# Optimization experiments

Hardware: AMD Instinct MI355X
Metric: run time of the kernel (lower is better)

## Reference

```python
import jax, jax.numpy as jnp
import numpy as np
from jax import lax

B, LEN_SEQ, D_MODEL, N_HEAD, FACTOR, D_FF = 16, 512, 512, 8, 5, 2048
EPS = 1e-5


def layer_norm(x):
    mu = x.mean(-1, keepdims=True)
    var = ((x - mu) ** 2).mean(-1, keepdims=True)
    return (x - mu) * lax.rsqrt(var + EPS)


def pos_encode(x):
    pos = jnp.arange(LEN_SEQ, dtype=jnp.float32)[:, None]
    div = jnp.exp(jnp.arange(0, D_MODEL, 2, dtype=jnp.float32) * (-np.log(10000.0) / D_MODEL))
    pe = jnp.zeros((LEN_SEQ, D_MODEL))
    pe = pe.at[:, 0::2].set(jnp.sin(pos * div)).at[:, 1::2].set(jnp.cos(pos * div))
    return x + pe[None]


def prob_attention(Q, K, V, rkey):
    # Q,K,V: [B,H,L,D]; Informer ProbSparse attention, mask_flag=False
    Bq, H, L_Q, D = Q.shape
    L_K = K.shape[2]
    U_part = min(FACTOR * int(np.ceil(np.log(L_K))), L_K)   # sampled keys per query
    u = min(FACTOR * int(np.ceil(np.log(L_Q))), L_Q)        # top queries kept
    idx = jax.random.randint(rkey, (L_Q, U_part), 0, L_K)
    K_samp = K[:, :, idx, :]                                # [B,H,L_Q,U_part,D]
    QK_samp = jnp.einsum('bhld,bhlsd->bhls', Q, K_samp)
    M = QK_samp.max(-1) - QK_samp.sum(-1) / L_K             # sparsity measure
    _, top = lax.top_k(M, u)                                # [B,H,u]
    Q_red = jnp.take_along_axis(Q, top[..., None], axis=2)  # [B,H,u,D]
    scores = jnp.einsum('bhud,bhkd->bhuk', Q_red, K) * (1.0 / np.sqrt(D))
    upd = jnp.einsum('bhuk,bhkd->bhud', jax.nn.softmax(scores, -1), V)
    ctx = jnp.broadcast_to(V.mean(2, keepdims=True), (Bq, H, L_Q, D))
    bi = jnp.arange(Bq)[:, None, None]
    hi = jnp.arange(H)[None, :, None]
    return ctx.at[bi, hi, top].set(upd)


def setup_inputs():
    key = jax.random.key(0)
    ks = jax.random.split(key, 12)
    s = 0.02
    d, f = D_MODEL, D_FF
    n = jax.random.normal
    return {
        'input_data': n(ks[0], (B, LEN_SEQ, d), jnp.float32),
        'Wq': n(ks[1], (d, d)) * s, 'bq': jnp.zeros((d,)),
        'Wk': n(ks[2], (d, d)) * s, 'bk': jnp.zeros((d,)),
        'Wv': n(ks[3], (d, d)) * s, 'bv': jnp.zeros((d,)),
        'Wo': n(ks[4], (d, d)) * s, 'bo': jnp.zeros((d,)),
        'enc_w1': n(ks[5], (d, f)) * s, 'enc_b1': jnp.zeros((f,)),
        'enc_w2': n(ks[6], (f, d)) * s, 'enc_b2': jnp.zeros((d,)),
        'dec_w1': n(ks[7], (d, f)) * s, 'dec_b1': jnp.zeros((f,)),
        'dec_w2': n(ks[8], (f, d)) * s, 'dec_b2': jnp.zeros((d,)),
        'dist_w': n(ks[9], (d, d, 3)) * s, 'dist_b': jnp.zeros((d,)),
        'out_w': n(ks[10], (d, 1)) * s, 'out_b': jnp.zeros((1,)),
    }


def reference(input_data, Wq, bq, Wk, bk, Wv, bv, Wo, bo,
              enc_w1, enc_b1, enc_w2, enc_b2,
              dec_w1, dec_b1, dec_w2, dec_b2,
              dist_w, dist_b, out_w, out_b):
    base = jax.random.key(42)

    def attn(q_in, k_in, v_in, i):
        Bq, L, _ = q_in.shape
        S = k_in.shape[1]
        Q = (q_in @ Wq + bq).reshape(Bq, L, N_HEAD, -1).transpose(0, 2, 1, 3)
        K = (k_in @ Wk + bk).reshape(Bq, S, N_HEAD, -1).transpose(0, 2, 1, 3)
        V = (v_in @ Wv + bv).reshape(Bq, S, N_HEAD, -1).transpose(0, 2, 1, 3)
        ctx = prob_attention(Q, K, V, jax.random.fold_in(base, i))
        return ctx.transpose(0, 2, 1, 3).reshape(Bq, L, -1) @ Wo + bo

    def encoder(x, i):
        x = layer_norm(x + attn(x, x, x, i))
        y = jax.nn.relu(x @ enc_w1 + enc_b1) @ enc_w2 + enc_b2
        return layer_norm(x + y)

    def distill(x):  # conv1d(circular) + batchnorm + ELU + maxpool(3,2,1)
        xc = x.transpose(0, 2, 1)                                   # [B,d,L]
        xp = jnp.concatenate([xc[..., -1:], xc, xc[..., :1]], -1)   # circular pad
        y = lax.conv_general_dilated(xp, dist_w, (1,), 'VALID',
                                     dimension_numbers=('NCH', 'OIH', 'NCH'))
        y = y + dist_b[None, :, None]
        mu = y.mean((0, 2), keepdims=True)
        var = ((y - mu) ** 2).mean((0, 2), keepdims=True)
        y = jax.nn.elu((y - mu) * lax.rsqrt(var + EPS))
        y = lax.reduce_window(y, -jnp.inf, lax.max, (1, 1, 3), (1, 1, 2),
                              [(0, 0), (0, 0), (1, 1)])
        return y.transpose(0, 2, 1)

    enc_inp = pos_encode(input_data)
    dec_inp = pos_encode(input_data)
    e = distill(encoder(enc_inp, 0))   # 512 -> 256
    e = distill(encoder(e, 1))         # 256 -> 128
    e = distill(encoder(e, 2))         # 128 -> 64
    # decoder (source DecoderLayer never applies its norms; dropout = identity in eval)
    out1 = dec_inp + attn(dec_inp, dec_inp, dec_inp, 3)
    out2 = out1 + attn(out1, e, e, 4)
    y = jax.nn.relu(out2 @ dec_w1 + dec_b1) @ dec_w2 + dec_b2
    out3 = y + out2
    return out3 @ out_w + out_b
```

## Files before the change

### kernel.cpp

```cpp
#include <hip/hip_runtime.h>
#include <cstdint>
#include <cmath>


#define HD __host__ __device__

typedef short short8 __attribute__((ext_vector_type(8)));
typedef float float4v __attribute__((ext_vector_type(4)));

typedef __attribute__((address_space(1))) const void gvoid;
typedef __attribute__((address_space(3))) void lvoid;

__device__ __forceinline__ void gl_lds16(const void* g, void* l) {
    __builtin_amdgcn_global_load_lds((gvoid*)g, (lvoid*)l, 16, 0, 0);
}

__device__ inline short f2bf(float f) {
    unsigned u = __float_as_uint(f);
    unsigned r = u + 0x7FFFu + ((u >> 16) & 1u);
    return (short)(r >> 16);
}

HD inline unsigned rotl32(unsigned x, int r) { return (x << r) | (x >> (32 - r)); }
HD inline void tfround(unsigned& x0, unsigned& x1, int r) {
    x0 += x1; x1 = rotl32(x1, r); x1 ^= x0;
}
HD inline void threefry2x32(unsigned k0, unsigned k1, unsigned c0, unsigned c1,
                            unsigned& o0, unsigned& o1) {
    unsigned ks2 = k0 ^ k1 ^ 0x1BD11BDAu;
    unsigned x0 = c0 + k0, x1 = c1 + k1;
    tfround(x0, x1, 13); tfround(x0, x1, 15); tfround(x0, x1, 26); tfround(x0, x1, 6);
    x0 += k1; x1 += ks2 + 1u;
    tfround(x0, x1, 17); tfround(x0, x1, 29); tfround(x0, x1, 16); tfround(x0, x1, 24);
    x0 += ks2; x1 += k0 + 2u;
    tfround(x0, x1, 13); tfround(x0, x1, 15); tfround(x0, x1, 26); tfround(x0, x1, 6);
    x0 += k0; x1 += k1 + 3u;
    tfround(x0, x1, 17); tfround(x0, x1, 29); tfround(x0, x1, 16); tfround(x0, x1, 24);
    x0 += k1; x1 += ks2 + 4u;
    tfround(x0, x1, 13); tfround(x0, x1, 15); tfround(x0, x1, 26); tfround(x0, x1, 6);
    x0 += ks2; x1 += k0 + 5u;
    o0 = x0; o1 = x1;
}


__global__ void pe_add_k(const float* __restrict__ in, float* __restrict__ out,
                         short* __restrict__ outb, int total8) {
    int t = blockIdx.x * 256 + threadIdx.x;
    if (t >= total8) return;
    int e = t * 8;
    int d0 = e & 511;
    int l = (e >> 9) & 511;
    float4 v0 = *(const float4*)(in + e);
    float4 v1 = *(const float4*)(in + e + 4);
    float vin[8] = {v0.x, v0.y, v0.z, v0.w, v1.x, v1.y, v1.z, v1.w};
    float r[8];
    #pragma unroll
    for (int p = 0; p < 4; p++) {
        int d = d0 + 2 * p;
        float div = expf((float)d * (-0.017988946039016f));
        float ang = (float)l * div;
        float s, c;
        sincosf(ang, &s, &c);
        r[2 * p] = vin[2 * p] + s;
        r[2 * p + 1] = vin[2 * p + 1] + c;
    }
    *(float4*)(out + e) = (float4){r[0], r[1], r[2], r[3]};
    *(float4*)(out + e + 4) = (float4){r[4], r[5], r[6], r[7]};
    short8 ob;
    #pragma unroll
    for (int p = 0; p < 8; p++) ob[p] = f2bf(r[p]);
    *(short8*)(outb + e) = ob;
}

__global__ __launch_bounds__(256) void wprep_k(
    const float* __restrict__ Wq, const float* __restrict__ Wk,
    const float* __restrict__ Wv, const float* __restrict__ Wo,
    const float* __restrict__ ew1, const float* __restrict__ ew2,
    const float* __restrict__ dw1, const float* __restrict__ dw2,
    short* __restrict__ WqkvT, short* __restrict__ WoT,
    short* __restrict__ e1T, short* __restrict__ e2T,
    short* __restrict__ d1T, short* __restrict__ d2T,
    const float* __restrict__ DW, short* __restrict__ W2T,
    const float* __restrict__ b0, const float* __restrict__ b1,
    const float* __restrict__ b2, float* __restrict__ bqkv) {
    int b = blockIdx.x;
    if (b < 5120) {
        const float* in; short* out; int K, N, tb;
        if (b < 1024) {
            int w = b >> 8; tb = b & 255;
            in = (w == 0) ? Wq : (w == 1) ? Wk : (w == 2) ? Wv : Wo;
            out = (w < 3) ? WqkvT + w * 512 * 512 : WoT;
            K = 512; N = 512;
        } else if (b < 2048) { in = ew1; out = e1T; K = 512; N = 2048; tb = b - 1024; }
        else if (b < 3072)   { in = ew2; out = e2T; K = 2048; N = 512; tb = b - 2048; }
        else if (b < 4096)   { in = dw1; out = d1T; K = 512; N = 2048; tb = b - 3072; }
        else                 { in = dw2; out = d2T; K = 2048; N = 512; tb = b - 4096; }
        int nbx = N >> 5;
        int k0 = (tb / nbx) << 5, n0 = (tb % nbx) << 5;
        __shared__ float tile[32][33];
        int c = threadIdx.x & 31, r0 = threadIdx.x >> 5;
        for (int rr = r0; rr < 32; rr += 8)
            tile[rr][c] = in[(size_t)(k0 + rr) * N + n0 + c];
        __syncthreads();
        for (int rr = r0; rr < 32; rr += 8)
            out[(size_t)(n0 + rr) * K + k0 + c] = f2bf(tile[c][rr]);
        return;
    }
    if (b < 8192) {
        int t = (b - 5120) * 256 + threadIdx.x;
        int kk = t % 1536;
        int o = t / 1536;
        int h = kk / 512, i = kk % 512;
        W2T[t] = f2bf(DW[(size_t)o * 1536 + i * 3 + h]);
        return;
    }
    int t = (b - 8192) * 256 + threadIdx.x;
    if (t < 1536)
        bqkv[t] = (t < 512) ? b0[t] : (t < 1024 ? b1[t - 512] : b2[t - 1024]);
}

__device__ inline void swizzle_bid(int bid, int nbx, int nby, int& bm, int& bn) {
    if ((nby & 7) == 0) {
        int stripe = nby >> 3;
        int x = bid & 7, w = bid >> 3;
        bn = w % nbx;
        bm = x * stripe + w / nbx;
    } else {
        bn = bid % nbx;
        bm = bid / nbx;
    }
}

__global__ __launch_bounds__(256) void gemm128_k(
    const short* __restrict__ A, const short* __restrict__ Bt,
    const float* __restrict__ bias, const float* __restrict__ res,
    float* __restrict__ C32, short* __restrict__ C16,
    int M, int N, int K, int relu, int ldC) {
    __shared__ short As[2][128 * 64];
    __shared__ short Bs[2][128 * 64];
    int tid = threadIdx.x;
    int wave = tid >> 6, lane = tid & 63;
    int wy = wave >> 1, wx = wave & 1;
    int rl = lane & 15, quad = lane >> 4;
    int bm, bn;
    swizzle_bid(blockIdx.x, N >> 7, M >> 7, bm, bn);
    bm <<= 7; bn <<= 7;

    int srow = (wave << 5) + (lane >> 2);
    int skol = (((lane & 3) ^ ((srow >> 1) & 3)) << 3);
    const short* ga0 = A + (size_t)(bm + srow) * K + skol;
    const short* ga1 = ga0 + (size_t)16 * K;
    const short* gb0 = Bt + (size_t)(bn + srow) * K + skol;
    const short* gb1 = gb0 + (size_t)16 * K;
    int lao = wave << 10;
    int ksw = (quad ^ ((rl >> 1) & 3)) << 3;

    float4v acc[4][4];
    #pragma unroll
    for (int i = 0; i < 4; i++)
        #pragma unroll
        for (int j = 0; j < 4; j++) acc[i][j] = (float4v){0.f, 0.f, 0.f, 0.f};

    int niter = K >> 6;
    auto stagePair = [&](int p, int bf) {
        int k0 = p << 6;
        gl_lds16(ga0 + k0, &As[bf][lao]);
        gl_lds16(ga1 + k0, &As[bf][lao + 512]);
        gl_lds16(gb0 + k0, &Bs[bf][lao]);
        gl_lds16(gb1 + k0, &Bs[bf][lao + 512]);
        gl_lds16(ga0 + k0 + 32, &As[bf][4096 + lao]);
        gl_lds16(ga1 + k0 + 32, &As[bf][4096 + lao + 512]);
        gl_lds16(gb0 + k0 + 32, &Bs[bf][4096 + lao]);
        gl_lds16(gb1 + k0 + 32, &Bs[bf][4096 + lao + 512]);
    };
    stagePair(0, 0);
    asm volatile("s_waitcnt vmcnt(0)" ::: "memory");
    __builtin_amdgcn_s_barrier();
    __builtin_amdgcn_sched_barrier(0);
    int cur = 0;
    for (int p = 0; p < niter; ++p) {
        if (p + 1 < niter) stagePair(p + 1, cur ^ 1);
        #pragma unroll
        for (int hh = 0; hh < 2; hh++) {
            const short* Ab = &As[cur][hh * 4096];
            const short* Bb = &Bs[cur][hh * 4096];
            short8 a[4], b[4];
            #pragma unroll
            for (int i = 0; i < 4; i++)
                a[i] = *(const short8*)&Ab[(wy * 64 + i * 16 + rl) * 32 + ksw];
            #pragma unroll
            for (int j = 0; j < 4; j++)
                b[j] = *(const short8*)&Bb[(wx * 64 + j * 16 + rl) * 32 + ksw];
            #pragma unroll
            for (int i = 0; i < 4; i++)
                #pragma unroll
                for (int j = 0; j < 4; j++)
                    acc[i][j] = __builtin_amdgcn_mfma_f32_16x16x32_bf16(a[i], b[j], acc[i][j], 0, 0, 0);
        }
        asm volatile("s_waitcnt vmcnt(0)" ::: "memory");
        __builtin_amdgcn_s_barrier();
        __builtin_amdgcn_sched_barrier(0);
        cur ^= 1;
    }
    #pragma unroll
    for (int i = 0; i < 4; i++) {
        #pragma unroll
        for (int r = 0; r < 4; r++) {
            int gm = bm + wy * 64 + i * 16 + quad * 4 + r;
            #pragma unroll
            for (int j = 0; j < 4; j++) {
                int gn = bn + wx * 64 + j * 16 + rl;
                float v = acc[i][j][r];
                if (bias) v += bias[gn];
                if (relu) v = fmaxf(v, 0.f);
                if (res) v += res[(size_t)gm * ldC + gn];
                if (C32) C32[(size_t)gm * ldC + gn] = v;
                if (C16) C16[(size_t)gm * ldC + gn] = f2bf(v);
            }
        }
    }
}

extern __shared__ short gls[];

__global__ __launch_bounds__(256) void gemm12864_k(
    const short* __restrict__ A, const short* __restrict__ Bt,
    const float* __restrict__ bias, const float* __restrict__ res,
    float* __restrict__ C32, short* __restrict__ C16,
    int M, int N, int K, int relu, int ldC) {
    int tid = threadIdx.x;
    int wave = tid >> 6, lane = tid & 63;
    int wy = wave >> 1, wx = wave & 1;
    int rl = lane & 15, quad = lane >> 4;
    int bm, bn;
    swizzle_bid(blockIdx.x, N >> 6, M >> 7, bm, bn);
    bm <<= 7; bn <<= 6;

    int arow = (wave << 5) + (lane >> 2);
    int brow = (wave << 4) + (lane >> 2);
    int ska = (((lane & 3) ^ ((arow >> 1) & 3)) << 3);
    int skb = (((lane & 3) ^ ((brow >> 1) & 3)) << 3);
    const short* ga0 = A + (size_t)(bm + arow) * K + ska;
    const short* ga1 = ga0 + (size_t)16 * K;
    const short* gb0 = Bt + (size_t)(bn + brow) * K + skb;
    int lao = wave << 10;
    int lbo = wave << 9;
    int ksw = (quad ^ ((rl >> 1) & 3)) << 3;

    float4v acc[4][2];
    #pragma unroll
    for (int i = 0; i < 4; i++)
        #pragma unroll
        for (int j = 0; j < 2; j++) acc[i][j] = (float4v){0.f, 0.f, 0.f, 0.f};

    int nt = K >> 5;
    int niter = nt >> 1;

    auto stageT = [&](int t, int bf) {
        int k0 = t << 5;
        short* Ab = gls + bf * 6144;
        short* Bb = Ab + 4096;
        gl_lds16(ga0 + k0, Ab + lao);
        gl_lds16(ga1 + k0, Ab + lao + 512);
        gl_lds16(gb0 + k0, Bb + lbo);
    };
    auto computeT = [&](int bf) {
        const short* Ab = gls + bf * 6144;
        const short* Bb = Ab + 4096;
        short8 a[4], b[2];
        #pragma unroll
        for (int i = 0; i < 4; i++)
            a[i] = *(const short8*)&Ab[(wy * 64 + i * 16 + rl) * 32 + ksw];
        #pragma unroll
        for (int j = 0; j < 2; j++)
            b[j] = *(const short8*)&Bb[(wx * 32 + j * 16 + rl) * 32 + ksw];
        #pragma unroll
        for (int i = 0; i < 4; i++)
            #pragma unroll
            for (int j = 0; j < 2; j++)
                acc[i][j] = __builtin_amdgcn_mfma_f32_16x16x32_bf16(a[i], b[j], acc[i][j], 0, 0, 0);
    };

    stageT(0, 0); stageT(1, 1);
    stageT(2, 2); stageT(3, 3);
    asm volatile("s_waitcnt vmcnt(6)" ::: "memory");
    __builtin_amdgcn_s_barrier();
    __builtin_amdgcn_sched_barrier(0);
    int q = 0;
    for (int p = 0; p < niter; ++p) {
        if (p + 2 < niter) {
            int s = q + 2; if (s >= 3) s -= 3;
            int t0 = (p + 2) << 1;
            stageT(t0, 2 * s);
            stageT(t0 + 1, 2 * s + 1);
        }
        computeT(2 * q);
        computeT(2 * q + 1);
        if (p + 2 < niter) {
            asm volatile("s_waitcnt vmcnt(6)" ::: "memory");
        } else {
            asm volatile("s_waitcnt vmcnt(0)" ::: "memory");
        }
        __builtin_amdgcn_s_barrier();
        __builtin_amdgcn_sched_barrier(0);
        q = (q == 2) ? 0 : q + 1;
    }
    #pragma unroll
    for (int i = 0; i < 4; i++) {
        #pragma unroll
        for (int r = 0; r < 4; r++) {
            int gm = bm + wy * 64 + i * 16 + quad * 4 + r;
            #pragma unroll
            for (int j = 0; j < 2; j++) {
                int gn = bn + wx * 32 + j * 16 + rl;
                float v = acc[i][j][r];
                if (bias) v += bias[gn];
                if (relu) v = fmaxf(v, 0.f);
                if (res) v += res[(size_t)gm * ldC + gn];
                if (C32) C32[(size_t)gm * ldC + gn] = v;
                if (C16) C16[(size_t)gm * ldC + gn] = f2bf(v);
            }
        }
    }
}

__global__ __launch_bounds__(256) void gemm64_k(
    const short* __restrict__ A, const short* __restrict__ Bt,
    const float* __restrict__ bias, const float* __restrict__ res,
    float* __restrict__ C32, short* __restrict__ C16,
    int M, int N, int K, int relu, int ldC) {
    __shared__ short As[2][64 * 32];
    __shared__ short Bs[2][64 * 32];
    int tid = threadIdx.x;
    int wave = tid >> 6, lane = tid & 63;
    int rl = lane & 15, quad = lane >> 4;
    int bm, bn;
    swizzle_bid(blockIdx.x, N >> 6, M >> 6, bm, bn);
    bm <<= 6; bn <<= 6;

    int srow = (wave << 4) + (lane >> 2);
    int skol = (((lane & 3) ^ ((srow >> 1) & 3)) << 3);
    const short* ga = A + (size_t)(bm + srow) * K + skol;
    const short* gb = Bt + (size_t)(bn + srow) * K + skol;
    int lof = wave << 9;
    int ksw = (quad ^ ((rl >> 1) & 3)) << 3;

    float4v acc[4];
    #pragma unroll
    for (int j = 0; j < 4; j++) acc[j] = (float4v){0.f, 0.f, 0.f, 0.f};

    int nsteps = K >> 5;
    auto stage = [&](int t, int bf) {
        int k0 = t << 5;
        gl_lds16(ga + k0, &As[bf][lof]);
        gl_lds16(gb + k0, &Bs[bf][lof]);
    };
    stage(0, 0);
    asm volatile("s_waitcnt vmcnt(0)" ::: "memory");
    __builtin_amdgcn_s_barrier();
    __builtin_amdgcn_sched_barrier(0);
    int cur = 0;
    for (int t = 0; t < nsteps; ++t) {
        if (t + 1 < nsteps) stage(t + 1, cur ^ 1);
        short8 a = *(const short8*)&As[cur][(wave * 16 + rl) * 32 + ksw];
        short8 b[4];
        #pragma unroll
        for (int j = 0; j < 4; j++)
            b[j] = *(const short8*)&Bs[cur][(j * 16 + rl) * 32 + ksw];
        #pragma unroll
        for (int j = 0; j < 4; j++)
            acc[j] = __builtin_amdgcn_mfma_f32_16x16x32_bf16(a, b[j], acc[j], 0, 0, 0);
        asm volatile("s_waitcnt vmcnt(0)" ::: "memory");
        __builtin_amdgcn_s_barrier();
        __builtin_amdgcn_sched_barrier(0);
        cur ^= 1;
    }
    #pragma unroll
    for (int r = 0; r < 4; r++) {
        int gm = bm + wave * 16 + quad * 4 + r;
        #pragma unroll
        for (int j = 0; j < 4; j++) {
            int gn = bn + j * 16 + rl;
            float v = acc[j][r];
            if (bias) v += bias[gn];
            if (relu) v = fmaxf(v, 0.f);
            if (res) v += res[(size_t)gm * ldC + gn];
            if (C32) C32[(size_t)gm * ldC + gn] = v;
            if (C16) C16[(size_t)gm * ldC + gn] = f2bf(v);
        }
    }
}

__global__ void ridx_k(unsigned k0, unsigned k1, int size, unsigned mask, int* __restrict__ idx) {
    int j = blockIdx.x * 256 + threadIdx.x;
    if (j >= size) return;
    unsigned o0, o1;
    threefry2x32(k0, k1, (unsigned)j, (unsigned)(j + size), o0, o1);
    idx[j] = (int)(o1 & mask);
}

extern __shared__ float kslab[];
__global__ __launch_bounds__(256) void msamp_lds_k(
    const float* __restrict__ Qp, const float* __restrict__ Kp,
    const int* __restrict__ idx, float* __restrict__ Mout,
    int LQ, int LK, int U, int ld) {
    int bid = blockIdx.x;
    int half = bid & 1;
    int bh = bid >> 1;
    int h = bh & 7, b = bh >> 3;
    const float* kbase = Kp + (size_t)b * LK * ld + h * 64;
    for (int t = threadIdx.x; t < LK * 16; t += 256) {
        int r = t >> 4, seg = t & 15;
        float4 v = *(const float4*)(kbase + (size_t)r * ld + seg * 4);
        float* dst = &kslab[r * 65 + seg * 4];
        dst[0] = v.x; dst[1] = v.y; dst[2] = v.z; dst[3] = v.w;
    }
    __syncthreads();
    int halfL = LQ >> 1;
    for (int li = threadIdx.x; li < halfL; li += 256) {
        int l = half * halfL + li;
        const float4* q = (const float4*)(Qp + (size_t)(b * LQ + l) * ld + h * 64);
        float qr[64];
        #pragma unroll
        for (int d4 = 0; d4 < 16; d4++) {
            float4 v = q[d4];
            qr[4 * d4] = v.x; qr[4 * d4 + 1] = v.y; qr[4 * d4 + 2] = v.z; qr[4 * d4 + 3] = v.w;
        }
        const int* ip = idx + l * U;
        float mx = -INFINITY, sm = 0.f;
        for (int s = 0; s < U; s++) {
            const float* kr = &kslab[ip[s] * 65];
            float acc = 0.f;
            #pragma unroll
            for (int d = 0; d < 64; d++) acc += qr[d] * kr[d];
            mx = fmaxf(mx, acc);
            sm += acc;
        }
        Mout[(size_t)bh * LQ + l] = mx - sm / (float)LK;
    }
}

__global__ void msamp_k(const float* __restrict__ Qp, const float* __restrict__ Kp,
                        const int* __restrict__ idx, float* __restrict__ Mout,
                        int LQ, int LK, int U, int ld) {
    int t = blockIdx.x * 256 + threadIdx.x;
    int total = 16 * 8 * LQ * 4;
    if (t >= total) return;
    int p = t & 3;
    int rest = t >> 2;
    int l = rest % LQ;
    int h = (rest / LQ) & 7;
    int b = rest / (LQ * 8);
    const float4* q = (const float4*)(Qp + ((size_t)(b * LQ + l) * ld + h * 64));
    const float* kb = Kp + ((size_t)b * LK * ld + h * 64);
    float4 qr[16];
    #pragma unroll
    for (int d = 0; d < 16; d++) qr[d] = q[d];
    float mx = -INFINITY, sm = 0.f;
    for (int s = p; s < U; s += 4) {
        const float4* kr = (const float4*)(kb + (size_t)idx[l * U + s] * ld);
        float acc = 0.f;
        #pragma unroll
        for (int d = 0; d < 16; d++) {
            float4 kv = kr[d];
            acc += qr[d].x * kv.x + qr[d].y * kv.y + qr[d].z * kv.z + qr[d].w * kv.w;
        }
        mx = fmaxf(mx, acc);
        sm += acc;
    }
    mx = fmaxf(mx, __shfl_xor(mx, 1));
    mx = fmaxf(mx, __shfl_xor(mx, 2));
    sm += __shfl_xor(sm, 1);
    sm += __shfl_xor(sm, 2);
    if (p == 0)
        Mout[(size_t)((b * 8) + h) * LQ + l] = mx - sm / (float)LK;
}

__global__ __launch_bounds__(256) void topk_k(const float* __restrict__ M,
                                              int* __restrict__ top, int LQ, int u) {
    int wave = threadIdx.x >> 6, lane = threadIdx.x & 63;
    int bh = blockIdx.x * 4 + wave;
    const float* m = M + (size_t)bh * LQ;
    float v[8];
    int id[8];
    #pragma unroll
    for (int s = 0; s < 8; s++) {
        int l = s * 64 + lane;
        if (l < LQ) { v[s] = m[l]; id[s] = l; }
        else        { v[s] = -INFINITY; id[s] = 0x7FFFFFFF; }
    }
    int* o = top + bh * u;
    for (int j = 0; j < u; j++) {
        float bv = v[0]; int bi = id[0];
        #pragma unroll
        for (int s = 1; s < 8; s++)
            if (v[s] > bv || (v[s] == bv && id[s] < bi)) { bv = v[s]; bi = id[s]; }
        #pragma unroll
        for (int off = 32; off > 0; off >>= 1) {
            float v2 = __shfl_xor(bv, off);
            int i2 = __shfl_xor(bi, off);
            if (v2 > bv || (v2 == bv && i2 < bi)) { bv = v2; bi = i2; }
        }
        if (lane == 0) o[j] = bi;
        int ws = bi >> 6, wl = bi & 63;
        #pragma unroll
        for (int s = 0; s < 8; s++)
            if (s == ws && lane == wl) v[s] = -INFINITY;
    }
}

__global__ __launch_bounds__(256) void vmean_k(const float* __restrict__ Vp,
                                               float* __restrict__ vm, int LK, int ld) {
    __shared__ float red[8][33];
    int b = blockIdx.y;
    int c0 = blockIdx.x * 32;
    int ci = threadIdx.x & 31, g = threadIdx.x >> 5;
    const float* base = Vp + (size_t)b * LK * ld + c0 + ci;
    float s = 0.f;
    for (int l = g; l < LK; l += 8) s += base[(size_t)l * ld];
    red[g][ci] = s;
    __syncthreads();
    if (threadIdx.x < 32) {
        float t = 0.f;
        #pragma unroll
        for (int g2 = 0; g2 < 8; g2++) t += red[g2][threadIdx.x];
        vm[b * 512 + c0 + threadIdx.x] = t / (float)LK;
    }
}

__global__ void ctx_fill_k(const float* __restrict__ vm, short* __restrict__ ctxb,
                           int LQ, int total8) {
    int t = blockIdx.x * 256 + threadIdx.x;
    if (t >= total8) return;
    int e = t * 8;
    int c = e & 511;
    int b = e / (LQ << 9);
    float4 v0 = *(const float4*)(vm + b * 512 + c);
    float4 v1 = *(const float4*)(vm + b * 512 + c + 4);
    float vv[8] = {v0.x, v0.y, v0.z, v0.w, v1.x, v1.y, v1.z, v1.w};
    short8 ob;
    #pragma unroll
    for (int p = 0; p < 8; p++) ob[p] = f2bf(vv[p]);
    *(short8*)(ctxb + e) = ob;
}

__global__ __launch_bounds__(256) void attn_flash_k(
    const float* __restrict__ Qp, const float* __restrict__ Kp, const float* __restrict__ Vp,
    const int* __restrict__ top, short* __restrict__ ctxb, int LQ, int LK, int u, int ld) {
    __shared__ float qs[18][64];
    __shared__ int ls[18];
    __shared__ float kv[64][65];
    __shared__ float sc[18][512];
    int bid = blockIdx.x;
    int chunk = bid & 1;
    int h = (bid >> 1) & 7;
    int b = bid >> 4;
    int CH = (u + 1) >> 1;
    int r0 = chunk * CH;
    int nr = min(CH, u - r0);
    int tid = threadIdx.x;
    int wave = tid >> 6, lane = tid & 63;

    if (tid < nr) ls[tid] = top[((b * 8) + h) * u + r0 + tid];
    __syncthreads();
    for (int t = tid; t < nr * 16; t += 256) {
        int r = t >> 4, seg = t & 15;
        float4 v = *(const float4*)(Qp + ((size_t)(b * LQ + ls[r])) * ld + h * 64 + seg * 4);
        float* dst = &qs[r][seg * 4];
        dst[0] = v.x; dst[1] = v.y; dst[2] = v.z; dst[3] = v.w;
    }

    int ntile = LK >> 6;
    const float* kbase = Kp + ((size_t)b * LK) * ld + h * 64;
    for (int T = 0; T < ntile; T++) {
        __syncthreads();
        #pragma unroll
        for (int it = 0; it < 4; it++) {
            int t = tid + it * 256;
            int kk = t >> 4, seg = t & 15;
            float4 v = *(const float4*)(kbase + (size_t)(T * 64 + kk) * ld + seg * 4);
            float* dst = &kv[kk][seg * 4];
            dst[0] = v.x; dst[1] = v.y; dst[2] = v.z; dst[3] = v.w;
        }
        __syncthreads();
        for (int p = tid; p < nr * 64; p += 256) {
            int r = p >> 6, kk = p & 63;
            float acc = 0.f;
            #pragma unroll
            for (int d = 0; d < 64; d++) acc += qs[r][d] * kv[kk][d];
            sc[r][T * 64 + kk] = acc * 0.125f;
        }
    }
    __syncthreads();
    for (int r = wave; r < nr; r += 4) {
        float mx = -INFINITY;
        for (int k = lane; k < LK; k += 64) mx = fmaxf(mx, sc[r][k]);
        #pragma unroll
        for (int o = 32; o > 0; o >>= 1) mx = fmaxf(mx, __shfl_xor(mx, o));
        float s = 0.f;
        for (int k = lane; k < LK; k += 64) {
            float e = expf(sc[r][k] - mx);
            sc[r][k] = e;
            s += e;
        }
        #pragma unroll
        for (int o = 32; o > 0; o >>= 1) s += __shfl_xor(s, o);
        float inv = 1.0f / s;
        for (int k = lane; k < LK; k += 64) sc[r][k] *= inv;
    }
    float acc[5];
    #pragma unroll
    for (int i = 0; i < 5; i++) acc[i] = 0.f;
    const float* vbase = Vp + ((size_t)b * LK) * ld + h * 64;
    for (int T = 0; T < ntile; T++) {
        __syncthreads();
        #pragma unroll
        for (int it = 0; it < 4; it++) {
            int t = tid + it * 256;
            int kk = t >> 4, seg = t & 15;
            float4 v = *(const float4*)(vbase + (size_t)(T * 64 + kk) * ld + seg * 4);
            float* dst = &kv[kk][seg * 4];
            dst[0] = v.x; dst[1] = v.y; dst[2] = v.z; dst[3] = v.w;
        }
        __syncthreads();
        int ri = 0;
        for (int r = wave; r < nr; r += 4, ri++) {
            float a = 0.f;
            #pragma unroll
            for (int kk = 0; kk < 64; kk++) a += sc[r][T * 64 + kk] * kv[kk][lane];
            acc[ri] += a;
        }
    }
    int ri = 0;
    for (int r = wave; r < nr; r += 4, ri++)
        ctxb[((size_t)(b * LQ + ls[r])) * 512 + h * 64 + lane] = f2bf(acc[ri]);
}

__global__ __launch_bounds__(256) void ln_k(const float* __restrict__ in,
                                            float* __restrict__ out, short* __restrict__ outb) {
    __shared__ float wred[8];
    int r = blockIdx.x;
    int tid = threadIdx.x;
    int wave = tid >> 6, lane = tid & 63;
    const float* x = in + (size_t)r * 512;
    float a = x[tid], b = x[tid + 256];
    float s = a + b;
    #pragma unroll
    for (int o = 32; o > 0; o >>= 1) s += __shfl_xor(s, o);
    if (lane == 0) wred[wave] = s;
    __syncthreads();
    float mu = (wred[0] + wred[1] + wred[2] + wred[3]) * (1.f / 512.f);
    float d1 = a - mu, d2 = b - mu;
    float q = d1 * d1 + d2 * d2;
    #pragma unroll
    for (int o = 32; o > 0; o >>= 1) q += __shfl_xor(q, o);
    if (lane == 0) wred[wave + 4] = q;
    __syncthreads();
    float inv = 1.0f / sqrtf((wred[4] + wred[5] + wred[6] + wred[7]) * (1.f / 512.f) + 1e-5f);
    float v1 = d1 * inv, v2 = d2 * inv;
    out[(size_t)r * 512 + tid] = v1;
    out[(size_t)r * 512 + tid + 256] = v2;
    if (outb) {
        outb[(size_t)r * 512 + tid] = f2bf(v1);
        outb[(size_t)r * 512 + tid + 256] = f2bf(v2);
    }
}

__global__ void xcat_k(const float* __restrict__ x, short* __restrict__ xc, int L, int total8) {
    int t = blockIdx.x * 256 + threadIdx.x;
    if (t >= total8) return;
    int e = t * 8;
    int i = e & 511;
    int q = e >> 9;
    int h = q % 3;
    int bt = q / 3;
    int tt = bt % L;
    int b = bt / L;
    int src = (tt + h - 1 + L) % L;
    const float* s = x + (size_t)(b * L + src) * 512 + i;
    float4 v0 = *(const float4*)s;
    float4 v1 = *(const float4*)(s + 4);
    float vv[8] = {v0.x, v0.y, v0.z, v0.w, v1.x, v1.y, v1.z, v1.w};
    short8 ob;
    #pragma unroll
    for (int p = 0; p < 8; p++) ob[p] = f2bf(vv[p]);
    *(short8*)(xc + e) = ob;
}

__global__ __launch_bounds__(256) void bnpart_k(const float* __restrict__ y,
                                                float* __restrict__ ps, float* __restrict__ pq,
                                                int rows) {
    int chunk = blockIdx.x;
    int rpc = rows >> 8;
    int r0 = chunk * rpc;
    int tid = threadIdx.x;
    float s0 = 0.f, s1 = 0.f, q0 = 0.f, q1 = 0.f;
    for (int r = r0; r < r0 + rpc; r++) {
        float a = y[(size_t)r * 512 + tid];
        float b = y[(size_t)r * 512 + tid + 256];
        s0 += a; q0 += a * a;
        s1 += b; q1 += b * b;
    }
    ps[chunk * 512 + tid] = s0;
    ps[chunk * 512 + tid + 256] = s1;
    pq[chunk * 512 + tid] = q0;
    pq[chunk * 512 + tid + 256] = q1;
}

__global__ void bnfin_k(const float* __restrict__ ps, const float* __restrict__ pq,
                        float* __restrict__ mu, float* __restrict__ var, int rows) {
    int o = blockIdx.x * 256 + threadIdx.x;
    if (o >= 512) return;
    float s = 0.f, q = 0.f;
    for (int c = 0; c < 256; c++) {
        s += ps[c * 512 + o];
        q += pq[c * 512 + o];
    }
    float m = s / (float)rows;
    mu[o] = m;
    var[o] = q / (float)rows - m * m;
}

__global__ void elu_pool_k(const float* __restrict__ y, const float* __restrict__ mu,
                           const float* __restrict__ var, float* __restrict__ out,
                           short* __restrict__ outb, int L, int total8) {
    int t = blockIdx.x * 256 + threadIdx.x;
    if (t >= total8) return;
    int e = t * 8;
    int o = e & 511;
    int tp = (e >> 9) % (L / 2);
    int b = (e >> 9) / (L / 2);
    float4 m0 = *(const float4*)(mu + o);
    float4 m1 = *(const float4*)(mu + o + 4);
    float4 g0 = *(const float4*)(var + o);
    float4 g1 = *(const float4*)(var + o + 4);
    float mm[8] = {m0.x, m0.y, m0.z, m0.w, m1.x, m1.y, m1.z, m1.w};
    float gg[8] = {g0.x, g0.y, g0.z, g0.w, g1.x, g1.y, g1.z, g1.w};
    float best[8];
    #pragma unroll
    for (int p = 0; p < 8; p++) best[p] = -INFINITY;
    #pragma unroll
    for (int dt = 0; dt < 3; dt++) {
        int tt = 2 * tp - 1 + dt;
        if (tt < 0 || tt >= L) continue;
        const float* row = y + (size_t)(b * L + tt) * 512 + o;
        float4 r0 = *(const float4*)row;
        float4 r1 = *(const float4*)(row + 4);
        float rr[8] = {r0.x, r0.y, r0.z, r0.w, r1.x, r1.y, r1.z, r1.w};
        #pragma unroll
        for (int p = 0; p < 8; p++) best[p] = fmaxf(best[p], rr[p]);
    }
    float res[8];
    short8 ob;
    #pragma unroll
    for (int p = 0; p < 8; p++) {
        float m = (best[p] - mm[p]) / sqrtf(gg[p] + 1e-5f);
        float r = m > 0.f ? m : expm1f(m);
        res[p] = r;
        ob[p] = f2bf(r);
    }
    *(float4*)(out + e) = (float4){res[0], res[1], res[2], res[3]};
    *(float4*)(out + e + 4) = (float4){res[4], res[5], res[6], res[7]};
    *(short8*)(outb + e) = ob;
}

__global__ void final_k(const float* __restrict__ x, const float* __restrict__ w,
                        const float* __restrict__ bb, float* __restrict__ out, int rows) {
    int gid = blockIdx.x * 256 + threadIdx.x;
    int wid = gid >> 6;
    int lane = gid & 63;
    if (wid >= rows) return;
    const float* xr = x + (size_t)wid * 512;
    float acc = 0.f;
    for (int k = lane; k < 512; k += 64) acc += xr[k] * w[k];
    for (int off = 32; off > 0; off >>= 1) acc += __shfl_down(acc, off);
    if (lane == 0) out[wid] = acc + bb[0];
}


static inline int iceil_log(int L) { return (int)ceil(log((double)L)); }
static inline int imin(int a, int b) { return a < b ? a : b; }

extern "C" void kernel_launch(void* const* d_in, const int* in_sizes, int n_in,
                              void* d_out, int out_size, void* d_ws, size_t ws_size,
                              hipStream_t stream) {
    const float* IN  = (const float*)d_in[0];
    const float* Wq  = (const float*)d_in[1];
    const float* bq  = (const float*)d_in[2];
    const float* Wk  = (const float*)d_in[3];
    const float* bk  = (const float*)d_in[4];
    const float* Wv  = (const float*)d_in[5];
    const float* bv  = (const float*)d_in[6];
    const float* Wo  = (const float*)d_in[7];
    const float* bo  = (const float*)d_in[8];
    const float* ew1 = (const float*)d_in[9];
    const float* eb1 = (const float*)d_in[10];
    const float* ew2 = (const float*)d_in[11];
    const float* eb2 = (const float*)d_in[12];
    const float* dw1 = (const float*)d_in[13];
    const float* db1 = (const float*)d_in[14];
    const float* dw2 = (const float*)d_in[15];
    const float* db2 = (const float*)d_in[16];
    const float* DW  = (const float*)d_in[17];
    const float* db  = (const float*)d_in[18];
    const float* ow  = (const float*)d_in[19];
    const float* ob  = (const float*)d_in[20];
    float* OUT = (float*)d_out;

    float* ws = (float*)d_ws;
    size_t off = 0;
    auto alloc = [&](size_t n) { float* p = ws + off; off += n; return p; };
    float* PE   = alloc(4194304);
    short* PEb  = (short*)alloc(2097152);
    float* QKV  = alloc(12582912);
    float* CTX  = alloc(4194304);
    short* CTXb = (short*)alloc(2097152);
    float* T1   = alloc(4194304);
    short* T1b  = (short*)alloc(2097152);
    float* XLN  = alloc(4194304);
    short* XLNb = (short*)alloc(2097152);
    float* T2   = alloc(4194304);
    short* T2b  = (short*)alloc(2097152);
    float* T3   = alloc(4194304);
    short* HIDb = (short*)alloc(8388608);
    float* D1   = alloc(2097152);
    short* D1b  = (short*)alloc(1048576);
    float* D2   = alloc(1048576);
    short* D2b  = (short*)alloc(524288);
    short* Ebb  = (short*)alloc(262144);
    float* Ebf  = alloc(524288);
    float* MB   = alloc(65536);
    float* VM   = alloc(8192);
    float* MU   = alloc(512);
    float* VARb = alloc(512);
    float* BQKV = alloc(1536);
    float* PS   = alloc(131072);
    float* PQ   = alloc(131072);
    int* IDX  = (int*)alloc(17920);
    int* TOPB = (int*)alloc(4480);
    short* WqkvT = (short*)alloc(393216);
    short* WoT   = (short*)alloc(131072);
    short* ew1T  = (short*)alloc(524288);
    short* ew2T  = (short*)alloc(524288);
    short* dw1T  = (short*)alloc(524288);
    short* dw2T  = (short*)alloc(524288);
    short* W2T   = (short*)alloc(393216);
    (void)ws_size; (void)n_in; (void)in_sizes; (void)out_size;

    static_assert(512 * 65 * 4 == 133120, "");
    hipError_t attr_ok = hipFuncSetAttribute(
        (const void*)msamp_lds_k, hipFuncAttributeMaxDynamicSharedMemorySize, 133120);
    hipError_t attr_g = hipFuncSetAttribute(
        (const void*)gemm12864_k, hipFuncAttributeMaxDynamicSharedMemorySize, 73728);

    auto gemm128 = [&](const short* A, const short* Bt, const float* bias, const float* res,
                       float* C32, short* C16, int M, int N, int K, int relu, int ldC) {
        gemm128_k<<<(N / 128) * (M / 128), 256, 0, stream>>>(A, Bt, bias, res, C32, C16,
                                                             M, N, K, relu, ldC);
    };
    auto gemm64 = [&](const short* A, const short* Bt, const float* bias, const float* res,
                      float* C32, short* C16, int M, int N, int K, int relu, int ldC) {
        if (attr_g == hipSuccess && M >= 8192 && (M & 127) == 0 && (N & 63) == 0 &&
            (K & 63) == 0) {
            gemm12864_k<<<(N / 64) * (M / 128), 256, 73728, stream>>>(A, Bt, bias, res,
                                                                      C32, C16, M, N, K,
                                                                      relu, ldC);
        } else {
            gemm64_k<<<(N / 64) * (M / 64), 256, 0, stream>>>(A, Bt, bias, res, C32, C16,
                                                              M, N, K, relu, ldC);
        }
    };

    auto attn = [&](const short* qinb, const short* kvinb, const float* resp,
                    float* out32, short* out16, int LQ, int LK, int ikey) {
        int Mq = 16 * LQ, Mk = 16 * LK;
        const int ld = 1536;
        float* Qp = QKV;
        float* Kp = QKV + 512;
        float* Vp = QKV + 1024;
        if (qinb == kvinb) {
            gemm128(qinb, WqkvT, BQKV, nullptr, QKV, nullptr, Mq, 1536, 512, 0, ld);
        } else {
            gemm64(qinb, WqkvT, BQKV, nullptr, QKV, nullptr, Mq, 512, 512, 0, ld);
            gemm64(kvinb, WqkvT + 512 * 512, BQKV + 512, nullptr, QKV + 512, nullptr,
                   Mk, 1024, 512, 0, ld);
        }
        int U = imin(5 * iceil_log(LK), LK);
        int u = imin(5 * iceil_log(LQ), LQ);
        unsigned rk0, rk1;
        threefry2x32(0u, 42u, 0u, (unsigned)ikey, rk0, rk1);
        int size = LQ * U;
        ridx_k<<<(size + 255) / 256, 256, 0, stream>>>(rk0, rk1, size, (unsigned)(LK - 1), IDX);
        size_t shbytes = (size_t)LK * 65 * 4;
        if (attr_ok == hipSuccess || shbytes <= 65536) {
            msamp_lds_k<<<16 * 8 * 2, 256, shbytes, stream>>>(Qp, Kp, IDX, MB, LQ, LK, U, ld);
        } else {
            int totM = 16 * 8 * LQ * 4;
            msamp_k<<<(totM + 255) / 256, 256, 0, stream>>>(Qp, Kp, IDX, MB, LQ, LK, U, ld);
        }
        topk_k<<<32, 256, 0, stream>>>(MB, TOPB, LQ, u);
        vmean_k<<<dim3(16, 16), 256, 0, stream>>>(Vp, VM, LK, ld);
        int totC8 = 16 * LQ * 512 / 8;
        ctx_fill_k<<<(totC8 + 255) / 256, 256, 0, stream>>>(VM, CTXb, LQ, totC8);
        attn_flash_k<<<16 * 8 * 2, 256, 0, stream>>>(Qp, Kp, Vp, TOPB, CTXb, LQ, LK, u, ld);
        gemm64(CTXb, WoT, bo, resp, out32, out16, Mq, 512, 512, 0, 512);
    };

    auto encoder = [&](const short* Xb, const float* X, int L, int ikey, float* OUTenc) {
        int M = 16 * L;
        attn(Xb, Xb, X, T1, nullptr, L, L, ikey);
        ln_k<<<M, 256, 0, stream>>>(T1, XLN, XLNb);
        gemm128(XLNb, ew1T, eb1, nullptr, nullptr, HIDb, M, 2048, 512, 1, 2048);
        gemm64(HIDb, ew2T, eb2, XLN, T2, nullptr, M, 512, 2048, 0, 512);
        ln_k<<<M, 256, 0, stream>>>(T2, OUTenc, nullptr);
    };

    auto distill = [&](const float* X, int L, float* OUTd, short* OUTdb) {
        int M = 16 * L;
        int tot8 = M * 1536 / 8;
        xcat_k<<<(tot8 + 255) / 256, 256, 0, stream>>>(X, HIDb, L, tot8);
        gemm64(HIDb, W2T, db, nullptr, CTX, nullptr, M, 512, 1536, 0, 512);
        bnpart_k<<<256, 256, 0, stream>>>(CTX, PS, PQ, M);
        bnfin_k<<<2, 256, 0, stream>>>(PS, PQ, MU, VARb, M);
        int toto8 = 16 * (L / 2) * 512 / 8;
        elu_pool_k<<<(toto8 + 255) / 256, 256, 0, stream>>>(CTX, MU, VARb, OUTd, OUTdb, L, toto8);
    };

    wprep_k<<<8198, 256, 0, stream>>>(Wq, Wk, Wv, Wo, ew1, ew2, dw1, dw2,
                                      WqkvT, WoT, ew1T, ew2T, dw1T, dw2T,
                                      DW, W2T, bq, bk, bv, BQKV);

    int totPE8 = 16 * 512 * 512 / 8;
    pe_add_k<<<(totPE8 + 255) / 256, 256, 0, stream>>>(IN, PE, PEb, totPE8);

    encoder(PEb, PE, 512, 0, T3); distill(T3, 512, D1, D1b);
    encoder(D1b, D1, 256, 1, T3); distill(T3, 256, D2, D2b);
    encoder(D2b, D2, 128, 2, T3); distill(T3, 128, Ebf, Ebb);

    attn(PEb, PEb, PE, T1, T1b, 512, 512, 3);
    attn(T1b, Ebb, T1, T2, T2b, 512, 64, 4);
    gemm128(T2b, dw1T, db1, nullptr, nullptr, HIDb, 8192, 2048, 512, 1, 2048);
    gemm64(HIDb, dw2T, db2, T2, T3, nullptr, 8192, 512, 2048, 0, 512);
    final_k<<<(8192 * 64) / 256, 256, 0, stream>>>(T3, ow, ob, OUT, 8192);
}
```

Before: 1.444 ms.

## Double-buffer K/V tiles in attention kernel and split dot-product accumulators

The attention kernel now double-buffers its K and V tiles in dynamic shared memory, prefetching the next tile into registers while the current one is computed. This is meant to hide global load latency behind the score and PV loops. Dot products in both the attention and sampled-score kernels are split into four independent accumulators to shorten the FMA dependency chain, which changes float summation order. Shared memory use grows to about 75KB per block, which may lower occupancy.

Result: slower. 1.534 ms (+6.2%).

```diff
diff --git a/kernel.cpp b/kernel.cpp
--- a/kernel.cpp
+++ b/kernel.cpp
@@ -222,6 +222,7 @@
 }
 
 extern __shared__ short gls[];
+extern __shared__ float kslab[];
 
 __global__ __launch_bounds__(256) void gemm12864_k(
     const short* __restrict__ A, const short* __restrict__ Bt,
@@ -399,7 +400,6 @@
     idx[j] = (int)(o1 & mask);
 }
 
-extern __shared__ float kslab[];
 __global__ __launch_bounds__(256) void msamp_lds_k(
     const float* __restrict__ Qp, const float* __restrict__ Kp,
     const int* __restrict__ idx, float* __restrict__ Mout,
@@ -430,9 +430,15 @@
         float mx = -INFINITY, sm = 0.f;
         for (int s = 0; s < U; s++) {
             const float* kr = &kslab[ip[s] * 65];
-            float acc = 0.f;
-            #pragma unroll
-            for (int d = 0; d < 64; d++) acc += qr[d] * kr[d];
+            float a0 = 0.f, a1 = 0.f, a2 = 0.f, a3 = 0.f;
+            #pragma unroll
+            for (int d = 0; d < 16; d++) {
+                a0 += qr[d] * kr[d];
+                a1 += qr[d + 16] * kr[d + 16];
+                a2 += qr[d + 32] * kr[d + 32];
+                a3 += qr[d + 48] * kr[d + 48];
+            }
+            float acc = (a0 + a1) + (a2 + a3);
             mx = fmaxf(mx, acc);
             sm += acc;
         }
@@ -547,10 +553,10 @@
 __global__ __launch_bounds__(256) void attn_flash_k(
     const float* __restrict__ Qp, const float* __restrict__ Kp, const float* __restrict__ Vp,
     const int* __restrict__ top, short* __restrict__ ctxb, int LQ, int LK, int u, int ld) {
-    __shared__ float qs[18][64];
-    __shared__ int ls[18];
-    __shared__ float kv[64][65];
-    __shared__ float sc[18][512];
+    float* qsf = kslab;
+    int* lsi = (int*)(kslab + 1152);
+    float* kvf = kslab + 1176;
+    float* scf = kslab + 1176 + 8320;
     int bid = blockIdx.x;
     int chunk = bid & 1;
     int h = (bid >> 1) & 7;
@@ -561,79 +567,156 @@
     int tid = threadIdx.x;
     int wave = tid >> 6, lane = tid & 63;
 
-    if (tid < nr) ls[tid] = top[((b * 8) + h) * u + r0 + tid];
+    if (tid < nr) lsi[tid] = top[((b * 8) + h) * u + r0 + tid];
     __syncthreads();
     for (int t = tid; t < nr * 16; t += 256) {
         int r = t >> 4, seg = t & 15;
-        float4 v = *(const float4*)(Qp + ((size_t)(b * LQ + ls[r])) * ld + h * 64 + seg * 4);
-        float* dst = &qs[r][seg * 4];
+        float4 v = *(const float4*)(Qp + ((size_t)(b * LQ + lsi[r])) * ld + h * 64 + seg * 4);
+        float* dst = &qsf[r * 64 + seg * 4];
         dst[0] = v.x; dst[1] = v.y; dst[2] = v.z; dst[3] = v.w;
     }
 
     int ntile = LK >> 6;
+    int kk0 = tid >> 4, sg4 = (tid & 15) * 4;
     const float* kbase = Kp + ((size_t)b * LK) * ld + h * 64;
+    const float* vbase = Vp + ((size_t)b * LK) * ld + h * 64;
+    float4 a0, a1, a2, a3;
+    auto LD = [&](const float* base, int T) {
+        const float* p = base + (size_t)(T * 64 + kk0) * ld + sg4;
+        a0 = *(const float4*)p;
+        a1 = *(const float4*)(p + (size_t)16 * ld);
+        a2 = *(const float4*)(p + (size_t)32 * ld);
+        a3 = *(const float4*)(p + (size_t)48 * ld);
+    };
+    auto ST = [&](int bf) {
+        float* d = &kvf[bf * 4160 + kk0 * 65 + sg4];
+        d[0] = a0.x; d[1] = a0.y; d[2] = a0.z; d[3] = a0.w; d += 16 * 65;
+        d[0] = a1.x; d[1] = a1.y; d[2] = a1.z; d[3] = a1.w; d += 16 * 65;
+        d[0] = a2.x; d[1] = a2.y; d[2] = a2.z; d[3] = a2.w; d += 16 * 65;
+        d[0] = a3.x; d[1] = a3.y; d[2] = a3.z; d[3] = a3.w;
+    };
+
+    LD(kbase, 0); ST(0);
+    __syncthreads();
+    int cur = 0;
     for (int T = 0; T < ntile; T++) {
-        __syncthreads();
-        #pragma unroll
-        for (int it = 0; it < 4; it++) {
-            int t = tid + it * 256;
-            int kk = t >> 4, seg = t & 15;
-            float4 v = *(const float4*)(kbase + (size_t)(T * 64 + kk) * ld + seg * 4);
-            float* dst = &kv[kk][seg * 4];
-            dst[0] = v.x; dst[1] = v.y; dst[2] = v.z; dst[3] = v.w;
-        }
-        __syncthreads();
+        if (T + 1 < ntile) LD(kbase, T + 1);
+        const float* kb = &kvf[cur * 4160];
         for (int p = tid; p < nr * 64; p += 256) {
             int r = p >> 6, kk = p & 63;
-            float acc = 0.f;
-            #pragma unroll
-            for (int d = 0; d < 64; d++) acc += qs[r][d] * kv[kk][d];
-            sc[r][T * 64 + kk] = acc * 0.125f;
-        }
-    }
-    __syncthreads();
+            const float* qr = &qsf[r * 64];
+            const float* kr = &kb[kk * 65];
+            float b0 = 0.f, b1 = 0.f, b2 = 0.f, b3 = 0.f;
+            #pragma unroll
+            for (int d = 0; d < 16; d++) {
+                b0 += qr[d] * kr[d];
+                b1 += qr[d + 16] * kr[d + 16];
+                b2 += qr[d + 32] * kr[d + 32];
+                b3 += qr[d + 48] * kr[d + 48];
+            }
+            scf[r * 512 + T * 64 + kk] = ((b0 + b1) + (b2 + b3)) * 0.125f;
+        }
+        __syncthreads();
+        if (T + 1 < ntile) ST(cur ^ 1);
+        __syncthreads();
+        cur ^= 1;
+    }
     for (int r = wave; r < nr; r += 4) {
         float mx = -INFINITY;
-        for (int k = lane; k < LK; k += 64) mx = fmaxf(mx, sc[r][k]);
+        for (int k = lane; k < LK; k += 64) mx = fmaxf(mx, scf[r * 512 + k]);
         #pragma unroll
         for (int o = 32; o > 0; o >>= 1) mx = fmaxf(mx, __shfl_xor(mx, o));
         float s = 0.f;
         for (int k = lane; k < LK; k += 64) {
-            float e = expf(sc[r][k] - mx);
-            sc[r][k] = e;
+            float e = expf(scf[r * 512 + k] - mx);
+            scf[r * 512 + k] = e;
             s += e;
         }
         #pragma unroll
         for (int o = 32; o > 0; o >>= 1) s += __shfl_xor(s, o);
         float inv = 1.0f / s;
-        for (int k = lane; k < LK; k += 64) sc[r][k] *= inv;
-    }
-    float acc[5];
-    #pragma unroll
-    for (int i = 0; i < 5; i++) acc[i] = 0.f;
-    const float* vbase = Vp + ((size_t)b * LK) * ld + h * 64;
+        for (int k = lane; k < LK; k += 64) scf[r * 512 + k] *= inv;
+    }
+    __syncthreads();
+
+    int rA = wave, rB = wave + 4, rC = wave + 8, rD = wave + 12, rE = wave + 16;
+    float accA = 0.f, accB = 0.f, accC = 0.f, accD = 0.f, accE = 0.f;
+    LD(vbase, 0); ST(0);
+    __syncthreads();
+    cur = 0;
     for (int T = 0; T < ntile; T++) {
+        if (T + 1 < ntile) LD(vbase, T + 1);
+        const float* vb = &kvf[cur * 4160];
+        if (rA < nr) {
+            const float* sr = &scf[rA * 512 + T * 64];
+            float b0 = 0.f, b1 = 0.f, b2 = 0.f, b3 = 0.f;
+            #pragma unroll
+            for (int kk = 0; kk < 16; kk++) {
+                b0 += sr[kk] * vb[kk * 65 + lane];
+                b1 += sr[kk + 16] * vb[(kk + 16) * 65 + lane];
+                b2 += sr[kk + 32] * vb[(kk + 32) * 65 + lane];
+                b3 += sr[kk + 48] * vb[(kk + 48) * 65 + lane];
+            }
+            accA += (b0 + b1) + (b2 + b3);
+        }
+        if (rB < nr) {
+            const float* sr = &scf[rB * 512 + T * 64];
+            float b0 = 0.f, b1 = 0.f, b2 = 0.f, b3 = 0.f;
+            #pragma unroll
+            for (int kk = 0; kk < 16; kk++) {
+                b0 += sr[kk] * vb[kk * 65 + lane];
+                b1 += sr[kk + 16] * vb[(kk + 16) * 65 + lane];
+                b2 += sr[kk + 32] * vb[(kk + 32) * 65 + lane];
+                b3 += sr[kk + 48] * vb[(kk + 48) * 65 + lane];
+            }
+            accB += (b0 + b1) + (b2 + b3);
+        }
+        if (rC < nr) {
+            const float* sr = &scf[rC * 512 + T * 64];
+            float b0 = 0.f, b1 = 0.f, b2 = 0.f, b3 = 0.f;
+            #pragma unroll
+            for (int kk = 0; kk < 16; kk++) {
+                b0 += sr[kk] * vb[kk * 65 + lane];
+                b1 += sr[kk + 16] * vb[(kk + 16) * 65 + lane];
+                b2 += sr[kk + 32] * vb[(kk + 32) * 65 + lane];
+                b3 += sr[kk + 48] * vb[(kk + 48) * 65 + lane];
+            }
+            accC += (b0 + b1) + (b2 + b3);
+        }
+        if (rD < nr) {
+            const float* sr = &scf[rD * 512 + T * 64];
+            float b0 = 0.f, b1 = 0.f, b2 = 0.f, b3 = 0.f;
+            #pragma unroll
+            for (int kk = 0; kk < 16; kk++) {
+                b0 += sr[kk] * vb[kk * 65 + lane];
+                b1 += sr[kk + 16] * vb[(kk + 16) * 65 + lane];
+                b2 += sr[kk + 32] * vb[(kk + 32) * 65 + lane];
+                b3 += sr[kk + 48] * vb[(kk + 48) * 65 + lane];
+            }
+            accD += (b0 + b1) + (b2 + b3);
+        }
+        if (rE < nr) {
+            const float* sr = &scf[rE * 512 + T * 64];
+            float b0 = 0.f, b1 = 0.f, b2 = 0.f, b3 = 0.f;
+            #pragma unroll
+            for (int kk = 0; kk < 16; kk++) {
+                b0 += sr[kk] * vb[kk * 65 + lane];
+                b1 += sr[kk + 16] * vb[(kk + 16) * 65 + lane];
+                b2 += sr[kk + 32] * vb[(kk + 32) * 65 + lane];
+                b3 += sr[kk + 48] * vb[(kk + 48) * 65 + lane];
+            }
+            accE += (b0 + b1) + (b2 + b3);
+        }
         __syncthreads();
-        #pragma unroll
-        for (int it = 0; it < 4; it++) {
-            int t = tid + it * 256;
-            int kk = t >> 4, seg = t & 15;
-            float4 v = *(const float4*)(vbase + (size_t)(T * 64 + kk) * ld + seg * 4);
-            float* dst = &kv[kk][seg * 4];
-            dst[0] = v.x; dst[1] = v.y; dst[2] = v.z; dst[3] = v.w;
-        }
+        if (T + 1 < ntile) ST(cur ^ 1);
         __syncthreads();
-        int ri = 0;
-        for (int r = wave; r < nr; r += 4, ri++) {
-            float a = 0.f;
-            #pragma unroll
-            for (int kk = 0; kk < 64; kk++) a += sc[r][T * 64 + kk] * kv[kk][lane];
-            acc[ri] += a;
-        }
-    }
-    int ri = 0;
-    for (int r = wave; r < nr; r += 4, ri++)
-        ctxb[((size_t)(b * LQ + ls[r])) * 512 + h * 64 + lane] = f2bf(acc[ri]);
+        cur ^= 1;
+    }
+    if (rA < nr) ctxb[((size_t)(b * LQ + lsi[rA])) * 512 + h * 64 + lane] = f2bf(accA);
+    if (rB < nr) ctxb[((size_t)(b * LQ + lsi[rB])) * 512 + h * 64 + lane] = f2bf(accB);
+    if (rC < nr) ctxb[((size_t)(b * LQ + lsi[rC])) * 512 + h * 64 + lane] = f2bf(accC);
+    if (rD < nr) ctxb[((size_t)(b * LQ + lsi[rD])) * 512 + h * 64 + lane] = f2bf(accD);
+    if (rE < nr) ctxb[((size_t)(b * LQ + lsi[rE])) * 512 + h * 64 + lane] = f2bf(accE);
 }
 
 __global__ __launch_bounds__(256) void ln_k(const float* __restrict__ in,
@@ -852,6 +935,10 @@
         (const void*)msamp_lds_k, hipFuncAttributeMaxDynamicSharedMemorySize, 133120);
     hipError_t attr_g = hipFuncSetAttribute(
         (const void*)gemm12864_k, hipFuncAttributeMaxDynamicSharedMemorySize, 73728);
+    const int ATTN_SHB = (1176 + 8320 + 9216) * 4;
+    hipError_t attr_a = hipFuncSetAttribute(
+        (const void*)attn_flash_k, hipFuncAttributeMaxDynamicSharedMemorySize, ATTN_SHB);
+    (void)attr_a;
 
     auto gemm128 = [&](const short* A, const short* Bt, const float* bias, const float* res,
                        float* C32, short* C16, int M, int N, int K, int relu, int ldC) {
@@ -902,7 +989,8 @@
         vmean_k<<<dim3(16, 16), 256, 0, stream>>>(Vp, VM, LK, ld);
         int totC8 = 16 * LQ * 512 / 8;
         ctx_fill_k<<<(totC8 + 255) / 256, 256, 0, stream>>>(VM, CTXb, LQ, totC8);
-        attn_flash_k<<<16 * 8 * 2, 256, 0, stream>>>(Qp, Kp, Vp, TOPB, CTXb, LQ, LK, u, ld);
+        attn_flash_k<<<16 * 8 * 2, 256, ATTN_SHB, stream>>>(Qp, Kp, Vp, TOPB, CTXb,
+                                                            LQ, LK, u, ld);
         gemm64(CTXb, WoT, bo, resp, out32, out16, Mq, 512, 512, 0, 512);
     };
 
```
